# Performance work log

Hardware: AMD Instinct MI355X
Metric: run time of the kernel (lower is better)

## Reference

```python
import jax, jax.numpy as jnp
import numpy as np

B, Cin, H, W = 8, 128, 64, 64
Cout, K, S, P = 128, 3, 1, 1
KK = K * K


def _conv(x, w, b=None):
    y = jax.lax.conv_general_dilated(
        x, w, window_strides=(S, S), padding=[(P, P), (P, P)],
        dimension_numbers=("NCHW", "OIHW", "NCHW"))
    if b is not None:
        y = y + b[None, :, None, None]
    return y


def setup_inputs() -> dict:
    key = jax.random.key(0)
    ks = jax.random.split(key, 6)
    x = jax.random.normal(ks[0], (B, Cin, H, W), jnp.float32)
    # offset/modulator convs are zero-init in the module; use small random
    # values so learned-offset sampling path is actually exercised.
    w_off = jax.random.normal(ks[1], (2 * KK, Cin, K, K), jnp.float32) * 0.01
    b_off = jax.random.normal(ks[2], (2 * KK,), jnp.float32) * 0.1
    w_mod = jax.random.normal(ks[3], (KK, Cin, K, K), jnp.float32) * 0.01
    b_mod = jax.random.normal(ks[4], (KK,), jnp.float32) * 0.1
    w_reg = jax.random.normal(ks[5], (Cout, Cin, K, K), jnp.float32) * (1.0 / np.sqrt(Cin * KK))
    return {"x": x, "w_off": w_off, "b_off": b_off,
            "w_mod": w_mod, "b_mod": b_mod, "w_reg": w_reg}


def _deform_conv2d(x, offset, mask, w_reg):
    # offset: [B, 2*KK, Hout, Wout] with (dy, dx) interleaved per tap (torchvision layout)
    Hout, Wout = offset.shape[2], offset.shape[3]
    off = offset.reshape(B, KK, 2, Hout, Wout)
    dy = off[:, :, 0].transpose(0, 2, 3, 1)  # [B,Hout,Wout,KK]
    dx = off[:, :, 1].transpose(0, 2, 3, 1)
    kh = (jnp.arange(KK) // K).astype(jnp.float32)
    kw = (jnp.arange(KK) % K).astype(jnp.float32)
    ho = jnp.arange(Hout, dtype=jnp.float32) * S - P
    wo = jnp.arange(Wout, dtype=jnp.float32) * S - P
    py = ho[None, :, None, None] + kh[None, None, None, :] + dy  # [B,Hout,Wout,KK]
    px = wo[None, None, :, None] + kw[None, None, None, :] + dx
    y0f = jnp.floor(py); x0f = jnp.floor(px)
    wy = (py - y0f)[..., None]; wx = (px - x0f)[..., None]
    y0 = y0f.astype(jnp.int32); x0 = x0f.astype(jnp.int32)
    x_bhwc = x.transpose(0, 2, 3, 1)  # [B,H,W,Cin]
    bidx = jnp.arange(B).reshape(B, 1, 1, 1)

    def gather(yi, xi):
        valid = ((yi >= 0) & (yi < H) & (xi >= 0) & (xi < W)).astype(x.dtype)
        v = x_bhwc[bidx, jnp.clip(yi, 0, H - 1), jnp.clip(xi, 0, W - 1)]
        return v * valid[..., None]  # [B,Hout,Wout,KK,Cin], zero outside

    v00 = gather(y0, x0)
    v01 = gather(y0, x0 + 1)
    v10 = gather(y0 + 1, x0)
    v11 = gather(y0 + 1, x0 + 1)
    val = (v00 * (1 - wy) * (1 - wx) + v01 * (1 - wy) * wx
           + v10 * wy * (1 - wx) + v11 * wy * wx)
    # modulated deformable conv v2: mask [B,KK,Hout,Wout]
    val = val * mask.transpose(0, 2, 3, 1)[..., None]
    # weighted accumulation over taps and input channels -> NCHW output
    return jnp.einsum("bhwkc,ock->bohw", val, w_reg.reshape(Cout, Cin, KK))


def reference(x, w_off, b_off, w_mod, b_mod, w_reg):
    offset = _conv(x, w_off, b_off)
    mask = 2.0 * jax.nn.sigmoid(_conv(x, w_mod, b_mod))
    return _deform_conv2d(x, offset, mask, w_reg)
```

## Files before the change

kernel.cpp:

```cpp
#include <hip/hip_runtime.h>
#include <hip/hip_bf16.h>
#include <math.h>

#define H 64
#define W 64
#define CIN 128
#define COUT 128
#define BATCH 8
#define NPIX (H*W)
#define PXT 32
#define AP  136
#define OAP 136

typedef __attribute__((ext_vector_type(8))) short bf16x8;
typedef __attribute__((ext_vector_type(4))) float f32x4;

static __device__ inline short f2bf(float f) {
  union { float f; unsigned u; } v; v.f = f;
  unsigned r = v.u + 0x7FFF + ((v.u >> 16) & 1);
  return (short)(r >> 16);
}
static __device__ inline float bf_lo(unsigned u) {
  union { unsigned u; float f; } v; v.u = u << 16; return v.f;
}
static __device__ inline float bf_hi(unsigned u) {
  union { unsigned u; float f; } v; v.u = u & 0xffff0000u; return v.f;
}

__global__ __launch_bounds__(256) void k_prep(const float* __restrict__ x,
    short* __restrict__ xbh,
    const float* __restrict__ w_off, const float* __restrict__ w_mod,
    short* __restrict__ wOM, const float* __restrict__ w_reg,
    short* __restrict__ wAs) {
  __shared__ float tile[32][65];
  int blk = blockIdx.x;
  int t = threadIdx.x;
  if (blk < 2048) {
    int cg = blk & 3, y = (blk >> 2) & 63, b = blk >> 8;
#pragma unroll
    for (int j = 0; j < 8; ++j) {
      int idx = t + j * 256;
      int ci = idx >> 6, xi = idx & 63;
      tile[ci][xi] = x[(((b * CIN + cg * 32 + ci) * H + y) * W) + xi];
    }
    __syncthreads();
#pragma unroll
    for (int j = 0; j < 8; ++j) {
      int idx = t + j * 256;
      int xi = idx >> 5, ci = idx & 31;
      xbh[((b * H + y) * W + xi) * CIN + cg * 32 + ci] = f2bf(tile[ci][xi]);
    }
  } else if (blk < 2048 + 144) {
    int e = (blk - 2048) * 256 + t;
    int tap = e >> 12, oc = (e >> 7) & 31, c = e & 127;
    float v = 0.f;
    if (oc < 18)      v = w_off[(oc * 128 + c) * 9 + tap];
    else if (oc < 27) v = w_mod[((oc - 18) * 128 + c) * 9 + tap];
    wOM[e] = f2bf(v);
  } else {
    int e = (blk - 2192) * 256 + t;
    int tap = e >> 14, oc = (e >> 7) & 127, c = e & 127;
    int kb = c >> 5, quad = (c >> 3) & 3, j = c & 7;
    int g = oc >> 4, l16 = oc & 15;
    int o = ((tap * 4 + kb) * 8 + g) * 512 + (quad * 16 + l16) * 8 + j;
    wAs[o] = f2bf(w_reg[(oc * 128 + c) * 9 + tap]);
  }
}

__global__ __launch_bounds__(256) void k_offmask(const short* __restrict__ xbh,
    const short* __restrict__ wOM, const float* __restrict__ b_off,
    const float* __restrict__ b_mod, float4* __restrict__ pym) {
  __shared__ __align__(16) short wa_s[32 * OAP];
  __shared__ __align__(16) short vs[64 * OAP];
  __shared__ float sc[32 * 68];

  int blk = blockIdx.x;
  int b = blk & 7, tile = blk >> 3;
  int pix0 = tile * 64;
  int t = threadIdx.x;
  int lane = t & 63, wv = t >> 6;
  int l16 = lane & 15, quad = lane >> 4;
  int cg = t & 15, pj = t >> 4;

  const short* xbb = xbh + (size_t)b * NPIX * CIN;
  f32x4 acc2[2] = {};

  for (int tap = 0; tap < 9; ++tap) {
    __syncthreads();
    {
      const float4* src = (const float4*)(wOM + tap * 4096);
#pragma unroll
      for (int j = 0; j < 2; ++j) {
        int e = t + j * 256;
        int oc = e >> 4, seg = e & 15;
        *(float4*)&wa_s[oc * OAP + seg * 8] = src[e];
      }
    }
    int dy = tap / 3 - 1, dx = tap % 3 - 1;
#pragma unroll
    for (int i = 0; i < 4; ++i) {
      int p = pj + i * 16;
      int gp = pix0 + p;
      int y = (gp >> 6) + dy, x = (gp & 63) + dx;
      bf16x8 v = {};
      if (y >= 0 && y < H && x >= 0 && x < W)
        v = *(const bf16x8*)&xbb[(size_t)((y << 6) + x) * CIN + cg * 8];
      *(bf16x8*)&vs[p * OAP + cg * 8] = v;
    }
    __syncthreads();
#pragma unroll
    for (int kb = 0; kb < 4; ++kb) {
      int kcol = kb * 32 + quad * 8;
      bf16x8 a0 = *(const bf16x8*)&wa_s[l16 * OAP + kcol];
      bf16x8 a1 = *(const bf16x8*)&wa_s[(16 + l16) * OAP + kcol];
      bf16x8 b0 = *(const bf16x8*)&vs[(wv * 16 + l16) * OAP + kcol];
      acc2[0] = __builtin_amdgcn_mfma_f32_16x16x32_bf16(a0, b0, acc2[0], 0, 0, 0);
      acc2[1] = __builtin_amdgcn_mfma_f32_16x16x32_bf16(a1, b0, acc2[1], 0, 0, 0);
    }
  }
  __syncthreads();
#pragma unroll
  for (int mt = 0; mt < 2; ++mt)
#pragma unroll
    for (int r = 0; r < 4; ++r) {
      int oc = mt * 16 + quad * 4 + r;
      int p  = wv * 16 + l16;
      sc[oc * 68 + p] = acc2[mt][r];
    }
  __syncthreads();
  for (int i = t; i < 64 * 9; i += 256) {
    int tap = i % 9, p = i / 9;
    float dyv = sc[(2 * tap) * 68 + p] + b_off[2 * tap];
    float dxv = sc[(2 * tap + 1) * 68 + p] + b_off[2 * tap + 1];
    float z   = sc[(18 + tap) * 68 + p] + b_mod[tap];
    float m = 2.f / (1.f + expf(-z));
    int gp = pix0 + p;
    float py = (float)((gp >> 6) - 1 + tap / 3) + dyv;
    float px = (float)((gp & 63) - 1 + tap % 3) + dxv;
    pym[(size_t)(b * NPIX + gp) * 9 + tap] = make_float4(py, px, m, 0.f);
  }
}

__global__ __launch_bounds__(512) void k_deform(const short* __restrict__ xbh,
    const float4* __restrict__ pym, const short* __restrict__ wAs,
    float* __restrict__ out) {
  __shared__ __align__(16) short vs[PXT * AP];
  __shared__ __align__(16) float pw[PXT * 9 * 4];
  __shared__ __align__(16) int   pa[PXT * 9 * 4];

  int blk = blockIdx.x;
  int b = blk & 7, tile = blk >> 3;
  int pix0 = tile * PXT;
  int t = threadIdx.x;
  int lane = t & 63;
  int wv = t >> 6;
  int ms = wv & 3, nh = wv >> 2;
  int l16 = lane & 15, quad = lane >> 4;

  for (int i = t; i < PXT * 9; i += 512) {
    float4 q = pym[(size_t)(b * NPIX + pix0 + i / 9) * 9 + (i % 9)];
    float py = q.x, pxx = q.y, m = q.z;
    float yf = floorf(py), xf = floorf(pxx);
    float wy = py - yf, wx = pxx - xf;
    int y0 = (int)yf, x0 = (int)xf;
    int y1 = y0 + 1, x1 = x0 + 1;
    float vy0 = (y0 >= 0 && y0 < H) ? 1.f : 0.f;
    float vy1 = (y1 >= 0 && y1 < H) ? 1.f : 0.f;
    float vx0 = (x0 >= 0 && x0 < W) ? 1.f : 0.f;
    float vx1 = (x1 >= 0 && x1 < W) ? 1.f : 0.f;
    int y0c = min(max(y0, 0), H - 1), y1c = min(max(y1, 0), H - 1);
    int x0c = min(max(x0, 0), W - 1), x1c = min(max(x1, 0), W - 1);
    *(float4*)&pw[i * 4] = make_float4((1.f - wy) * (1.f - wx) * m * vy0 * vx0,
                                       (1.f - wy) * wx * m * vy0 * vx1,
                                       wy * (1.f - wx) * m * vy1 * vx0,
                                       wy * wx * m * vy1 * vx1);
    *(int4*)&pa[i * 4] = make_int4(((y0c << 6) + x0c) << 7,
                                   ((y0c << 6) + x1c) << 7,
                                   ((y1c << 6) + x0c) << 7,
                                   ((y1c << 6) + x1c) << 7);
  }

  int cq = t & 31, pxsub = (t >> 5) & 1, grp = t >> 6;
  int c0 = cq * 4;
  const short* xbB = xbh + (size_t)b * NPIX * CIN;

  f32x4 acc[2] = {};

  for (int tap = 0; tap < 9; ++tap) {
    __syncthreads();

    const short* wtap = wAs + tap * 16384;
    bf16x8 af0[4], af1[4];
#pragma unroll
    for (int kb = 0; kb < 4; ++kb) {
      af0[kb] = *(const bf16x8*)&wtap[(kb * 8 + ms * 2) * 512 + lane * 8];
      af1[kb] = *(const bf16x8*)&wtap[(kb * 8 + ms * 2 + 1) * 512 + lane * 8];
    }

#pragma unroll
    for (int i = 0; i < 2; ++i) {
      int p = grp * 4 + i * 2 + pxsub;
      int idx = (p * 9 + tap) * 4;
      float4 wq = *(const float4*)&pw[idx];
      int4 aa = *(const int4*)&pa[idx];
      uint2 u00 = *(const uint2*)&xbB[aa.x + c0];
      uint2 u01 = *(const uint2*)&xbB[aa.y + c0];
      uint2 u10 = *(const uint2*)&xbB[aa.z + c0];
      uint2 u11 = *(const uint2*)&xbB[aa.w + c0];
      float s0 = wq.x * bf_lo(u00.x), s1 = wq.x * bf_hi(u00.x);
      float s2 = wq.x * bf_lo(u00.y), s3 = wq.x * bf_hi(u00.y);
      s0 = fmaf(wq.y, bf_lo(u01.x), s0); s1 = fmaf(wq.y, bf_hi(u01.x), s1);
      s2 = fmaf(wq.y, bf_lo(u01.y), s2); s3 = fmaf(wq.y, bf_hi(u01.y), s3);
      s0 = fmaf(wq.z, bf_lo(u10.x), s0); s1 = fmaf(wq.z, bf_hi(u10.x), s1);
      s2 = fmaf(wq.z, bf_lo(u10.y), s2); s3 = fmaf(wq.z, bf_hi(u10.y), s3);
      s0 = fmaf(wq.w, bf_lo(u11.x), s0); s1 = fmaf(wq.w, bf_hi(u11.x), s1);
      s2 = fmaf(wq.w, bf_lo(u11.y), s2); s3 = fmaf(wq.w, bf_hi(u11.y), s3);
      __hip_bfloat162 h2a = __float22bfloat162_rn(make_float2(s0, s1));
      __hip_bfloat162 h2b = __float22bfloat162_rn(make_float2(s2, s3));
      uint2 packed;
      packed.x = *(unsigned*)&h2a;
      packed.y = *(unsigned*)&h2b;
      *(uint2*)&vs[p * AP + c0] = packed;
    }
    __syncthreads();

#pragma unroll
    for (int kb = 0; kb < 4; ++kb) {
      int kcol = kb * 32 + quad * 8;
      bf16x8 b0 = *(const bf16x8*)&vs[(nh * 16 + l16) * AP + kcol];
      acc[0] = __builtin_amdgcn_mfma_f32_16x16x32_bf16(af0[kb], b0, acc[0], 0, 0, 0);
      acc[1] = __builtin_amdgcn_mfma_f32_16x16x32_bf16(af1[kb], b0, acc[1], 0, 0, 0);
    }
  }

  int oc_base = ms * 32;
#pragma unroll
  for (int mt = 0; mt < 2; ++mt)
#pragma unroll
    for (int r = 0; r < 4; ++r) {
      int oc = oc_base + mt * 16 + quad * 4 + r;
      int px = nh * 16 + l16;
      out[(size_t)(b * COUT + oc) * NPIX + pix0 + px] = acc[mt][r];
    }
}

extern "C" void kernel_launch(void* const* d_in, const int* in_sizes, int n_in,
                              void* d_out, int out_size, void* d_ws, size_t ws_size,
                              hipStream_t stream) {
  const float* x     = (const float*)d_in[0];
  const float* w_off = (const float*)d_in[1];
  const float* b_off = (const float*)d_in[2];
  const float* w_mod = (const float*)d_in[3];
  const float* b_mod = (const float*)d_in[4];
  const float* w_reg = (const float*)d_in[5];

  short* xbh  = (short*)d_ws;
  float* pym  = (float*)(xbh + 4194304);
  short* wAs  = (short*)(pym + 1179648);
  short* wOM  = wAs + 147456;
  float* out  = (float*)d_out;

  k_prep<<<dim3(2768), 256, 0, stream>>>(x, xbh, w_off, w_mod, wOM,
                                         w_reg, wAs);
  k_offmask<<<dim3(512), 256, 0, stream>>>(
      xbh, wOM, b_off, b_mod, (float4*)pym);
  k_deform<<<dim3(NPIX / PXT * BATCH), 512, 0, stream>>>(
      xbh, (const float4*)pym, wAs, out);
}
```

Baseline: 130.8 us.

## Fuse offset/mask convolution into deform kernel, dropping intermediate sampling buffer

Removes the separate offset/mask kernel and computes the offset and modulator convolution inside the deform kernel. Each wave handles one tap via MFMA with weights in a swizzled fragment layout, and partial sums are reduced across waves through shared memory. This drops one launch and the global write and read of the per-tap sampling buffer. In exchange it adds a 32 KB shared reduction buffer that may lower occupancy, and only one wave has a second tap, so that phase is unevenly loaded.

```diff
diff --git a/kernel.cpp b/kernel.cpp
--- a/kernel.cpp
+++ b/kernel.cpp
@@ -10,7 +10,6 @@
 #define NPIX (H*W)
 #define PXT 32
 #define AP  136
-#define OAP 136
 
 typedef __attribute__((ext_vector_type(8))) short bf16x8;
 typedef __attribute__((ext_vector_type(4))) float f32x4;
@@ -30,7 +29,7 @@
 __global__ __launch_bounds__(256) void k_prep(const float* __restrict__ x,
     short* __restrict__ xbh,
     const float* __restrict__ w_off, const float* __restrict__ w_mod,
-    short* __restrict__ wOM, const float* __restrict__ w_reg,
+    short* __restrict__ wOMs, const float* __restrict__ w_reg,
     short* __restrict__ wAs) {
   __shared__ float tile[32][65];
   int blk = blockIdx.x;
@@ -56,7 +55,10 @@
     float v = 0.f;
     if (oc < 18)      v = w_off[(oc * 128 + c) * 9 + tap];
     else if (oc < 27) v = w_mod[((oc - 18) * 128 + c) * 9 + tap];
-    wOM[e] = f2bf(v);
+    int kb = c >> 5, quad = (c >> 3) & 3, j = c & 7;
+    int g = oc >> 4, l16 = oc & 15;
+    int o = ((tap * 4 + kb) * 2 + g) * 512 + (quad * 16 + l16) * 8 + j;
+    wOMs[o] = f2bf(v);
   } else {
     int e = (blk - 2192) * 256 + t;
     int tap = e >> 14, oc = (e >> 7) & 127, c = e & 127;
@@ -67,83 +69,11 @@
   }
 }
 
-__global__ __launch_bounds__(256) void k_offmask(const short* __restrict__ xbh,
-    const short* __restrict__ wOM, const float* __restrict__ b_off,
-    const float* __restrict__ b_mod, float4* __restrict__ pym) {
-  __shared__ __align__(16) short wa_s[32 * OAP];
-  __shared__ __align__(16) short vs[64 * OAP];
-  __shared__ float sc[32 * 68];
-
-  int blk = blockIdx.x;
-  int b = blk & 7, tile = blk >> 3;
-  int pix0 = tile * 64;
-  int t = threadIdx.x;
-  int lane = t & 63, wv = t >> 6;
-  int l16 = lane & 15, quad = lane >> 4;
-  int cg = t & 15, pj = t >> 4;
-
-  const short* xbb = xbh + (size_t)b * NPIX * CIN;
-  f32x4 acc2[2] = {};
-
-  for (int tap = 0; tap < 9; ++tap) {
-    __syncthreads();
-    {
-      const float4* src = (const float4*)(wOM + tap * 4096);
-#pragma unroll
-      for (int j = 0; j < 2; ++j) {
-        int e = t + j * 256;
-        int oc = e >> 4, seg = e & 15;
-        *(float4*)&wa_s[oc * OAP + seg * 8] = src[e];
-      }
-    }
-    int dy = tap / 3 - 1, dx = tap % 3 - 1;
-#pragma unroll
-    for (int i = 0; i < 4; ++i) {
-      int p = pj + i * 16;
-      int gp = pix0 + p;
-      int y = (gp >> 6) + dy, x = (gp & 63) + dx;
-      bf16x8 v = {};
-      if (y >= 0 && y < H && x >= 0 && x < W)
-        v = *(const bf16x8*)&xbb[(size_t)((y << 6) + x) * CIN + cg * 8];
-      *(bf16x8*)&vs[p * OAP + cg * 8] = v;
-    }
-    __syncthreads();
-#pragma unroll
-    for (int kb = 0; kb < 4; ++kb) {
-      int kcol = kb * 32 + quad * 8;
-      bf16x8 a0 = *(const bf16x8*)&wa_s[l16 * OAP + kcol];
-      bf16x8 a1 = *(const bf16x8*)&wa_s[(16 + l16) * OAP + kcol];
-      bf16x8 b0 = *(const bf16x8*)&vs[(wv * 16 + l16) * OAP + kcol];
-      acc2[0] = __builtin_amdgcn_mfma_f32_16x16x32_bf16(a0, b0, acc2[0], 0, 0, 0);
-      acc2[1] = __builtin_amdgcn_mfma_f32_16x16x32_bf16(a1, b0, acc2[1], 0, 0, 0);
-    }
-  }
-  __syncthreads();
-#pragma unroll
-  for (int mt = 0; mt < 2; ++mt)
-#pragma unroll
-    for (int r = 0; r < 4; ++r) {
-      int oc = mt * 16 + quad * 4 + r;
-      int p  = wv * 16 + l16;
-      sc[oc * 68 + p] = acc2[mt][r];
-    }
-  __syncthreads();
-  for (int i = t; i < 64 * 9; i += 256) {
-    int tap = i % 9, p = i / 9;
-    float dyv = sc[(2 * tap) * 68 + p] + b_off[2 * tap];
-    float dxv = sc[(2 * tap + 1) * 68 + p] + b_off[2 * tap + 1];
-    float z   = sc[(18 + tap) * 68 + p] + b_mod[tap];
-    float m = 2.f / (1.f + expf(-z));
-    int gp = pix0 + p;
-    float py = (float)((gp >> 6) - 1 + tap / 3) + dyv;
-    float px = (float)((gp & 63) - 1 + tap % 3) + dxv;
-    pym[(size_t)(b * NPIX + gp) * 9 + tap] = make_float4(py, px, m, 0.f);
-  }
-}
-
 __global__ __launch_bounds__(512) void k_deform(const short* __restrict__ xbh,
-    const float4* __restrict__ pym, const short* __restrict__ wAs,
+    const short* __restrict__ wOMs, const float* __restrict__ b_off,
+    const float* __restrict__ b_mod, const short* __restrict__ wAs,
     float* __restrict__ out) {
+  __shared__ float red[8 * 1024];
   __shared__ __align__(16) short vs[PXT * AP];
   __shared__ __align__(16) float pw[PXT * 9 * 4];
   __shared__ __align__(16) int   pa[PXT * 9 * 4];
@@ -154,20 +84,71 @@
   int t = threadIdx.x;
   int lane = t & 63;
   int wv = t >> 6;
-  int ms = wv & 3, nh = wv >> 2;
   int l16 = lane & 15, quad = lane >> 4;
 
+  const short* xbB = xbh + (size_t)b * NPIX * CIN;
+
+  {
+    f32x4 acc_o[2][2] = {};
+    for (int tap = wv; tap < 9; tap += 8) {
+      const short* wt = wOMs + tap * 4096;
+      int dy = tap / 3 - 1, dx = tap % 3 - 1;
+      int lin[2], val[2];
+#pragma unroll
+      for (int nt = 0; nt < 2; ++nt) {
+        int gp = pix0 + nt * 16 + l16;
+        int y = (gp >> 6) + dy, x = (gp & 63) + dx;
+        int ok = ((unsigned)y < H) && ((unsigned)x < W);
+        val[nt] = ok;
+        lin[nt] = ok ? ((y << 6) + x) : 0;
+      }
+#pragma unroll
+      for (int kb = 0; kb < 4; ++kb) {
+        bf16x8 a0 = *(const bf16x8*)&wt[(kb * 2 + 0) * 512 + lane * 8];
+        bf16x8 a1 = *(const bf16x8*)&wt[(kb * 2 + 1) * 512 + lane * 8];
+#pragma unroll
+        for (int nt = 0; nt < 2; ++nt) {
+          bf16x8 bv = *(const bf16x8*)&xbB[(size_t)lin[nt] * CIN + kb * 32 + quad * 8];
+          if (!val[nt]) bv = (bf16x8){};
+          acc_o[0][nt] = __builtin_amdgcn_mfma_f32_16x16x32_bf16(a0, bv, acc_o[0][nt], 0, 0, 0);
+          acc_o[1][nt] = __builtin_amdgcn_mfma_f32_16x16x32_bf16(a1, bv, acc_o[1][nt], 0, 0, 0);
+        }
+      }
+    }
+#pragma unroll
+    for (int mt = 0; mt < 2; ++mt)
+#pragma unroll
+      for (int nt = 0; nt < 2; ++nt)
+#pragma unroll
+        for (int r = 0; r < 4; ++r) {
+          int oc = mt * 16 + quad * 4 + r;
+          int px = nt * 16 + l16;
+          red[wv * 1024 + oc * 32 + px] = acc_o[mt][nt][r];
+        }
+  }
+  __syncthreads();
+
   for (int i = t; i < PXT * 9; i += 512) {
-    float4 q = pym[(size_t)(b * NPIX + pix0 + i / 9) * 9 + (i % 9)];
-    float py = q.x, pxx = q.y, m = q.z;
+    int tap = i % 9, p = i / 9;
+    float dyv = b_off[2 * tap], dxv = b_off[2 * tap + 1], z = b_mod[tap];
+#pragma unroll
+    for (int w = 0; w < 8; ++w) {
+      dyv += red[w * 1024 + (2 * tap) * 32 + p];
+      dxv += red[w * 1024 + (2 * tap + 1) * 32 + p];
+      z   += red[w * 1024 + (18 + tap) * 32 + p];
+    }
+    float m = 2.f / (1.f + expf(-z));
+    int gp = pix0 + p;
+    float py = (float)((gp >> 6) - 1 + tap / 3) + dyv;
+    float pxx = (float)((gp & 63) - 1 + tap % 3) + dxv;
     float yf = floorf(py), xf = floorf(pxx);
     float wy = py - yf, wx = pxx - xf;
     int y0 = (int)yf, x0 = (int)xf;
     int y1 = y0 + 1, x1 = x0 + 1;
-    float vy0 = (y0 >= 0 && y0 < H) ? 1.f : 0.f;
-    float vy1 = (y1 >= 0 && y1 < H) ? 1.f : 0.f;
-    float vx0 = (x0 >= 0 && x0 < W) ? 1.f : 0.f;
-    float vx1 = (x1 >= 0 && x1 < W) ? 1.f : 0.f;
+    float vy0 = ((unsigned)y0 < H) ? 1.f : 0.f;
+    float vy1 = ((unsigned)y1 < H) ? 1.f : 0.f;
+    float vx0 = ((unsigned)x0 < W) ? 1.f : 0.f;
+    float vx1 = ((unsigned)x1 < W) ? 1.f : 0.f;
     int y0c = min(max(y0, 0), H - 1), y1c = min(max(y1, 0), H - 1);
     int x0c = min(max(x0, 0), W - 1), x1c = min(max(x1, 0), W - 1);
     *(float4*)&pw[i * 4] = make_float4((1.f - wy) * (1.f - wx) * m * vy0 * vx0,
@@ -180,9 +161,9 @@
                                    ((y1c << 6) + x1c) << 7);
   }
 
+  int ms = wv & 3, nh = wv >> 2;
   int cq = t & 31, pxsub = (t >> 5) & 1, grp = t >> 6;
   int c0 = cq * 4;
-  const short* xbB = xbh + (size_t)b * NPIX * CIN;
 
   f32x4 acc[2] = {};
 
@@ -255,15 +236,12 @@
   const float* w_reg = (const float*)d_in[5];
 
   short* xbh  = (short*)d_ws;
-  float* pym  = (float*)(xbh + 4194304);
-  short* wAs  = (short*)(pym + 1179648);
-  short* wOM  = wAs + 147456;
+  short* wAs  = xbh + 4194304;
+  short* wOMs = wAs + 147456;
   float* out  = (float*)d_out;
 
-  k_prep<<<dim3(2768), 256, 0, stream>>>(x, xbh, w_off, w_mod, wOM,
+  k_prep<<<dim3(2768), 256, 0, stream>>>(x, xbh, w_off, w_mod, wOMs,
                                          w_reg, wAs);
-  k_offmask<<<dim3(512), 256, 0, stream>>>(
-      xbh, wOM, b_off, b_mod, (float4*)pym);
   k_deform<<<dim3(NPIX / PXT * BATCH), 512, 0, stream>>>(
-      xbh, (const float4*)pym, wAs, out);
-}
+      xbh, wOMs, b_off, b_mod, wAs, out);
+}
```

Result: no change. 131.2 us (+0.3%).
